# Kernel tuning notes

Measured on AMD Instinct MI355X. Metric: run time of the kernel, lower is better.

Reference implementation:

```python
import jax, jax.numpy as jnp
import numpy as np

SEQ, BATCH, IN_DIM, HID, OUT = 512, 256, 300, 256, 2


def setup_inputs() -> dict:
    key = jax.random.key(0)
    ks = jax.random.split(key, 7)
    s_ih = 1.0 / np.sqrt(HID)
    return {
        "x": jax.random.normal(ks[0], (SEQ, BATCH, IN_DIM), jnp.float32),
        "W_ih": jax.random.uniform(ks[1], (HID, IN_DIM), jnp.float32, -s_ih, s_ih),
        "W_hh": jax.random.uniform(ks[2], (HID, HID), jnp.float32, -s_ih, s_ih),
        "b_ih": jax.random.uniform(ks[3], (HID,), jnp.float32, -s_ih, s_ih),
        "b_hh": jax.random.uniform(ks[4], (HID,), jnp.float32, -s_ih, s_ih),
        "W_fc": jax.random.uniform(ks[5], (OUT, HID), jnp.float32, -s_ih, s_ih),
        "b_fc": jax.random.uniform(ks[6], (OUT,), jnp.float32, -s_ih, s_ih),
    }


def reference(x, W_ih, W_hh, b_ih, b_hh, W_fc, b_fc):
    # Precompute input projection for all timesteps at once: [T, B, H]
    xp = jnp.einsum('tbi,hi->tbh', x, W_ih) + b_ih + b_hh

    def step(h, xt):
        h_new = jnp.tanh(xt + h @ W_hh.T)
        return h_new, None

    h0 = jnp.zeros((x.shape[1], W_hh.shape[0]), x.dtype)
    hT, _ = jax.lax.scan(step, h0, xp)  # hT: [B, H]
    # Dropout(0.3) is identity in eval mode.
    logits = hT @ W_fc.T + b_fc  # [B, 2]
    return jax.nn.log_softmax(logits, axis=-1)
```

## Files before the change

kernel.cpp:

```cpp
#include <hip/hip_runtime.h>
#include <hip/hip_bf16.h>
#include <cstdint>
#include <cstddef>

#define SEQ 512
#define BATCH 256
#define IN_DIM 300
#define HID 256

typedef __attribute__((ext_vector_type(8))) short bf16x8;
typedef __attribute__((ext_vector_type(4))) float f32x4;

__device__ __forceinline__ float bitsf(unsigned int u) {
  union { unsigned int u; float f; } v; v.u = u; return v.f;
}
__device__ __forceinline__ unsigned int pk2(float a, float b) {
  union { __hip_bfloat162 h2; unsigned int u; } p;
  p.h2 = __float22bfloat162_rn(make_float2(a, b));
  return p.u;
}
__device__ __forceinline__ bf16x8 cvt8(float a0,float a1,float a2,float a3,
                                       float a4,float a5,float a6,float a7) {
  union { __hip_bfloat162 h2[4]; bf16x8 v; } c;
  c.h2[0] = __float22bfloat162_rn(make_float2(a0, a1));
  c.h2[1] = __float22bfloat162_rn(make_float2(a2, a3));
  c.h2[2] = __float22bfloat162_rn(make_float2(a4, a5));
  c.h2[3] = __float22bfloat162_rn(make_float2(a6, a7));
  return c.v;
}

__global__ __launch_bounds__(256) void gemm_xp(const float* __restrict__ x,
    const float* __restrict__ W_ih, const float* __restrict__ b_ih,
    const float* __restrict__ b_hh, unsigned int* __restrict__ xp2)
{
  __shared__ unsigned short a_lds[64][40];
  __shared__ unsigned short w_lds[256][40];
  const int tid  = threadIdx.x;
  const int wave = tid >> 6;
  const int lane = tid & 63;
  const int l15  = lane & 15;
  const int quad = lane >> 4;
  const long m0 = (long)blockIdx.x * 64;

  f32x4 acc[4][4];
  #pragma unroll
  for (int mt = 0; mt < 4; ++mt)
    #pragma unroll
    for (int nt = 0; nt < 4; ++nt) acc[mt][nt] = (f32x4){0.f, 0.f, 0.f, 0.f};

  const int ar = tid >> 2;
  const int ac = (tid & 3) * 8;

  float av[8];
  float4 wv[8];
  {
    const float* src = x + (size_t)(m0 + ar) * IN_DIM + ac;
    float2 p0 = *(const float2*)(src + 0);
    float2 p1 = *(const float2*)(src + 2);
    float2 p2 = *(const float2*)(src + 4);
    float2 p3 = *(const float2*)(src + 6);
    av[0]=p0.x; av[1]=p0.y; av[2]=p1.x; av[3]=p1.y;
    av[4]=p2.x; av[5]=p2.y; av[6]=p3.x; av[7]=p3.y;
    #pragma unroll
    for (int i = 0; i < 8; ++i) {
      int e = tid + i * 256;
      wv[i] = *(const float4*)(W_ih + (e >> 3) * IN_DIM + (e & 7) * 4);
    }
  }

  for (int kc = 0; kc < 10; ++kc) {
    *(bf16x8*)&a_lds[ar][ac] = cvt8(av[0],av[1],av[2],av[3],av[4],av[5],av[6],av[7]);
    #pragma unroll
    for (int i = 0; i < 8; ++i) {
      int e = tid + i * 256;
      union { unsigned int u[2]; uint2 d; } pk;
      pk.u[0] = pk2(wv[i].x, wv[i].y);
      pk.u[1] = pk2(wv[i].z, wv[i].w);
      *(uint2*)&w_lds[e >> 3][(e & 7) * 4] = pk.d;
    }
    __syncthreads();
    if (kc < 9) {
      const int k0 = (kc + 1) * 32;
      const float* src = x + (size_t)(m0 + ar) * IN_DIM + (k0 + ac);
      if (k0 + ac + 8 <= IN_DIM) {
        float2 p0 = *(const float2*)(src + 0);
        float2 p1 = *(const float2*)(src + 2);
        float2 p2 = *(const float2*)(src + 4);
        float2 p3 = *(const float2*)(src + 6);
        av[0]=p0.x; av[1]=p0.y; av[2]=p1.x; av[3]=p1.y;
        av[4]=p2.x; av[5]=p2.y; av[6]=p3.x; av[7]=p3.y;
      } else {
        #pragma unroll
        for (int j = 0; j < 8; ++j) av[j] = (k0 + ac + j < IN_DIM) ? src[j] : 0.f;
      }
      #pragma unroll
      for (int i = 0; i < 8; ++i) {
        int e = tid + i * 256;
        int kk = k0 + (e & 7) * 4;
        wv[i] = (kk + 4 <= IN_DIM)
              ? *(const float4*)(W_ih + (e >> 3) * IN_DIM + kk)
              : make_float4(0.f, 0.f, 0.f, 0.f);
      }
    }
    bf16x8 afr[4], bfr[4];
    #pragma unroll
    for (int mt = 0; mt < 4; ++mt)
      afr[mt] = *(const bf16x8*)&a_lds[mt*16 + l15][quad*8];
    #pragma unroll
    for (int nt = 0; nt < 4; ++nt)
      bfr[nt] = *(const bf16x8*)&w_lds[wave*64 + nt*16 + l15][quad*8];
    #pragma unroll
    for (int mt = 0; mt < 4; ++mt)
      #pragma unroll
      for (int nt = 0; nt < 4; ++nt)
        acc[mt][nt] = __builtin_amdgcn_mfma_f32_16x16x32_bf16(afr[mt], bfr[nt], acc[mt][nt], 0, 0, 0);
    __syncthreads();
  }
  const int t = (int)(blockIdx.x >> 2);
  const float kb0 = 2.0f * (b_ih[wave*64 +  0 + l15] + b_hh[wave*64 +  0 + l15]);
  const float kb1 = 2.0f * (b_ih[wave*64 + 16 + l15] + b_hh[wave*64 + 16 + l15]);
  const float kb2 = 2.0f * (b_ih[wave*64 + 32 + l15] + b_hh[wave*64 + 32 + l15]);
  const float kb3 = 2.0f * (b_ih[wave*64 + 48 + l15] + b_hh[wave*64 + 48 + l15]);
  #pragma unroll
  for (int mt = 0; mt < 4; ++mt) {
    const int g = ((int)(blockIdx.x & 3))*16 + mt*4 + quad;
    const size_t base = ((size_t)t*64 + g)*512;
    #pragma unroll
    for (int r = 0; r < 4; ++r) {
      unsigned int d0 = pk2(fmaf(2.0f, acc[mt][0][r], kb0), fmaf(2.0f, acc[mt][1][r], kb1));
      unsigned int d1 = pk2(fmaf(2.0f, acc[mt][2][r], kb2), fmaf(2.0f, acc[mt][3][r], kb3));
      xp2[base + (wave*2    )*64 + r*16 + l15] = d0;
      xp2[base + (wave*2 + 1)*64 + r*16 + l15] = d1;
    }
  }
}

__global__ __launch_bounds__(512) void rnn_scan(const float* __restrict__ W_hh,
    const unsigned int* __restrict__ xp2, float* __restrict__ hT)
{
  __shared__ alignas(16) unsigned short hbuf[2][4 * 272];
  const int tid  = threadIdx.x;
  const int wave = tid >> 6;
  const int lane = tid & 63;
  const int l15  = lane & 15;
  const int quad = lane >> 4;
  const int g = blockIdx.x;
  const int c0 = wave * 32;

  bf16x8 wf[2][8];
  #pragma unroll
  for (int nt = 0; nt < 2; ++nt) {
    const int n = c0 + nt*16 + l15;
    #pragma unroll
    for (int kc = 0; kc < 8; ++kc) {
      const float* src = W_hh + n*HID + kc*32 + quad*4;
      float4 p0 = *(const float4*)src;
      float4 p1 = *(const float4*)(src + 16);
      wf[nt][kc] = cvt8(p0.x,p1.x,p0.y,p1.y,p0.z,p1.z,p0.w,p1.w);
    }
  }

  const int abase = (l15 & 3) * 272 + quad * 8;
  const int wofs  = quad * 272 + wave * 32 + l15 * 2;

  for (int i = tid; i < 4 * 272; i += 512) hbuf[0][i] = 0;

  const unsigned int* xbase = xp2 + (size_t)g * 512 + tid;

  __syncthreads();

  unsigned int xq[32];
  for (int tc = 0; tc < SEQ / 32; ++tc) {
    const unsigned int* pb = xbase + (size_t)tc * 32 * 32768;
    #pragma unroll
    for (int j = 0; j < 32; ++j)
      xq[j] = pb[(size_t)j * 32768];
    #pragma unroll
    for (int j = 0; j < 32; ++j) {
      const int cur = j & 1;
      bf16x8 afr[8];
      #pragma unroll
      for (int kc = 0; kc < 8; ++kc)
        afr[kc] = *(const bf16x8*)&hbuf[cur][abase + kc*32];
      f32x4 c00 = (f32x4){0.f,0.f,0.f,0.f}, c01 = c00, c10 = c00, c11 = c00;
      #pragma unroll
      for (int kc = 0; kc < 8; kc += 2) {
        c00 = __builtin_amdgcn_mfma_f32_16x16x32_bf16(afr[kc],   wf[0][kc],   c00, 0, 0, 0);
        c10 = __builtin_amdgcn_mfma_f32_16x16x32_bf16(afr[kc],   wf[1][kc],   c10, 0, 0, 0);
        c01 = __builtin_amdgcn_mfma_f32_16x16x32_bf16(afr[kc+1], wf[0][kc+1], c01, 0, 0, 0);
        c11 = __builtin_amdgcn_mfma_f32_16x16x32_bf16(afr[kc+1], wf[1][kc+1], c11, 0, 0, 0);
      }
      const bool qb0 = (quad & 1) != 0, qb1 = (quad & 2) != 0;
      float a0 = qb1 ? (qb0 ? c00[3]+c01[3] : c00[2]+c01[2])
                     : (qb0 ? c00[1]+c01[1] : c00[0]+c01[0]);
      float a1 = qb1 ? (qb0 ? c10[3]+c11[3] : c10[2]+c11[2])
                     : (qb0 ? c10[1]+c11[1] : c10[0]+c11[0]);
      float xv0 = bitsf(xq[j] << 16);
      float xv1 = bitsf(xq[j] & 0xffff0000u);
      float y0 = fmaf(2.0f, a0, xv0);
      float y1 = fmaf(2.0f, a1, xv1);
      float h0 = fmaf(-2.0f, __builtin_amdgcn_rcpf(__expf(y0) + 1.0f), 1.0f);
      float h1 = fmaf(-2.0f, __builtin_amdgcn_rcpf(__expf(y1) + 1.0f), 1.0f);
      if (j < 31 || tc < SEQ/32 - 1) {
        *(unsigned int*)&hbuf[1 - cur][wofs] = pk2(h0, h1);
      } else {
        hT[(size_t)(g*4 + quad) * HID + c0 + l15]      = h0;
        hT[(size_t)(g*4 + quad) * HID + c0 + 16 + l15] = h1;
      }
      __syncthreads();
    }
  }
}

__global__ __launch_bounds__(64) void fc_head(const float* __restrict__ hT,
    const float* __restrict__ W_fc, const float* __restrict__ b_fc,
    float* __restrict__ out)
{
  const int b = blockIdx.x;
  const int l = threadIdx.x;
  float s0 = 0.f, s1 = 0.f;
  #pragma unroll
  for (int j0 = 0; j0 < HID; j0 += 64) {
    float h = hT[(size_t)b * HID + j0 + l];
    s0 += h * W_fc[j0 + l];
    s1 += h * W_fc[HID + j0 + l];
  }
  #pragma unroll
  for (int off = 32; off > 0; off >>= 1) {
    s0 += __shfl_xor(s0, off, 64);
    s1 += __shfl_xor(s1, off, 64);
  }
  if (l == 0) {
    float l0 = s0 + b_fc[0], l1 = s1 + b_fc[1];
    float m = fmaxf(l0, l1);
    float lse = m + logf(expf(l0 - m) + expf(l1 - m));
    out[b*2 + 0] = l0 - lse;
    out[b*2 + 1] = l1 - lse;
  }
}

extern "C" void kernel_launch(void* const* d_in, const int* in_sizes, int n_in,
                              void* d_out, int out_size, void* d_ws, size_t ws_size,
                              hipStream_t stream) {
  const float* x    = (const float*)d_in[0];
  const float* W_ih = (const float*)d_in[1];
  const float* W_hh = (const float*)d_in[2];
  const float* b_ih = (const float*)d_in[3];
  const float* b_hh = (const float*)d_in[4];
  const float* W_fc = (const float*)d_in[5];
  const float* b_fc = (const float*)d_in[6];
  float* out = (float*)d_out;

  const size_t xp_bytes = (size_t)SEQ * BATCH * HID * 2;
  const size_t ht_bytes = (size_t)BATCH * HID * 4;
  if (ws_size < xp_bytes + ht_bytes) return;

  char* ws = (char*)d_ws;
  unsigned int* xp2 = (unsigned int*)ws;
  float*        hT  = (float*)(ws + xp_bytes);

  hipLaunchKernelGGL(gemm_xp,  dim3(2048), dim3(256), 0, stream, x, W_ih, b_ih, b_hh, xp2);
  hipLaunchKernelGGL(rnn_scan, dim3(64),   dim3(512), 0, stream, W_hh, xp2, hT);
  hipLaunchKernelGGL(fc_head,  dim3(BATCH), dim3(64), 0, stream, hT, W_fc, b_fc, out);
}
```

Before: 509.4 us.

## Halve scan waves per block, four N-tiles per wave, pre-permuted bf16 W_hh

The recurrent scan now uses 4 waves of 256 threads instead of 8 waves of 512. Each wave computes 64 hidden columns using four N-tiles, and it loads 8-byte xp chunks and writes 8-byte h chunks to LDS. A new pre-kernel converts W_hh to bf16 in a permuted layout so the scan loads its weight fragments with single vector loads. The aim is to cut per-step barrier cost across fewer waves and widen memory accesses. In exchange each wave has a longer serial MFMA chain and higher register pressure (32 weight fragments).

```diff
diff --git a/kernel.cpp b/kernel.cpp
--- a/kernel.cpp
+++ b/kernel.cpp
@@ -13,6 +13,11 @@
 
 __device__ __forceinline__ float bitsf(unsigned int u) {
   union { unsigned int u; float f; } v; v.u = u; return v.f;
+}
+__device__ __forceinline__ unsigned short f2bf(float f) {
+  union { float f; unsigned int u; } v; v.f = f;
+  unsigned int u = v.u;
+  return (unsigned short)((u + 0x7fffu + ((u >> 16) & 1u)) >> 16);
 }
 __device__ __forceinline__ unsigned int pk2(float a, float b) {
   union { __hip_bfloat162 h2; unsigned int u; } p;
@@ -29,9 +34,17 @@
   return c.v;
 }
 
+__global__ __launch_bounds__(256) void conv_whh(const float* __restrict__ W_hh,
+                                                unsigned short* __restrict__ w_perm) {
+  int idx = blockIdx.x * 256 + threadIdx.x;
+  int n = idx >> 8, P = idx & 255;
+  int k = (P & 192) + 16 * (P & 3) + ((P >> 2) & 15);
+  w_perm[idx] = f2bf(W_hh[n * 256 + k]);
+}
+
 __global__ __launch_bounds__(256) void gemm_xp(const float* __restrict__ x,
     const float* __restrict__ W_ih, const float* __restrict__ b_ih,
-    const float* __restrict__ b_hh, unsigned int* __restrict__ xp2)
+    const float* __restrict__ b_hh, uint2* __restrict__ xpv)
 {
   __shared__ unsigned short a_lds[64][40];
   __shared__ unsigned short w_lds[256][40];
@@ -124,88 +137,91 @@
   #pragma unroll
   for (int mt = 0; mt < 4; ++mt) {
     const int g = ((int)(blockIdx.x & 3))*16 + mt*4 + quad;
-    const size_t base = ((size_t)t*64 + g)*512;
+    const size_t base = ((size_t)t*64 + g)*256;
     #pragma unroll
     for (int r = 0; r < 4; ++r) {
-      unsigned int d0 = pk2(fmaf(2.0f, acc[mt][0][r], kb0), fmaf(2.0f, acc[mt][1][r], kb1));
-      unsigned int d1 = pk2(fmaf(2.0f, acc[mt][2][r], kb2), fmaf(2.0f, acc[mt][3][r], kb3));
-      xp2[base + (wave*2    )*64 + r*16 + l15] = d0;
-      xp2[base + (wave*2 + 1)*64 + r*16 + l15] = d1;
-    }
-  }
-}
-
-__global__ __launch_bounds__(512) void rnn_scan(const float* __restrict__ W_hh,
-    const unsigned int* __restrict__ xp2, float* __restrict__ hT)
+      uint2 d;
+      d.x = pk2(fmaf(2.0f, acc[mt][0][r], kb0), fmaf(2.0f, acc[mt][1][r], kb1));
+      d.y = pk2(fmaf(2.0f, acc[mt][2][r], kb2), fmaf(2.0f, acc[mt][3][r], kb3));
+      xpv[base + wave*64 + r*16 + l15] = d;
+    }
+  }
+}
+
+__global__ __launch_bounds__(256, 1) void rnn_scan(
+    const unsigned short* __restrict__ w_perm,
+    const uint2* __restrict__ xpv, float* __restrict__ hT)
 {
-  __shared__ alignas(16) unsigned short hbuf[2][4 * 272];
+  __shared__ alignas(16) unsigned short hbuf[2][4][272];
   const int tid  = threadIdx.x;
   const int wave = tid >> 6;
   const int lane = tid & 63;
   const int l15  = lane & 15;
   const int quad = lane >> 4;
   const int g = blockIdx.x;
-  const int c0 = wave * 32;
-
-  bf16x8 wf[2][8];
-  #pragma unroll
-  for (int nt = 0; nt < 2; ++nt) {
+  const int c0 = wave * 64;
+  const int m = l15 & 3;
+
+  bf16x8 wf[4][8];
+  #pragma unroll
+  for (int nt = 0; nt < 4; ++nt) {
     const int n = c0 + nt*16 + l15;
     #pragma unroll
-    for (int kc = 0; kc < 8; ++kc) {
-      const float* src = W_hh + n*HID + kc*32 + quad*4;
-      float4 p0 = *(const float4*)src;
-      float4 p1 = *(const float4*)(src + 16);
-      wf[nt][kc] = cvt8(p0.x,p1.x,p0.y,p1.y,p0.z,p1.z,p0.w,p1.w);
-    }
-  }
-
-  const int abase = (l15 & 3) * 272 + quad * 8;
-  const int wofs  = quad * 272 + wave * 32 + l15 * 2;
-
-  for (int i = tid; i < 4 * 272; i += 512) hbuf[0][i] = 0;
-
-  const unsigned int* xbase = xp2 + (size_t)g * 512 + tid;
+    for (int kc = 0; kc < 8; ++kc)
+      wf[nt][kc] = *(const bf16x8*)(w_perm + (size_t)n*256 + kc*32 + quad*8);
+  }
+
+  for (int i = tid; i < 4 * 272; i += 256) (&hbuf[0][0][0])[i] = 0;
+
+  const uint2* xb = xpv + (size_t)g * 256 + tid;
 
   __syncthreads();
 
-  unsigned int xq[32];
-  for (int tc = 0; tc < SEQ / 32; ++tc) {
-    const unsigned int* pb = xbase + (size_t)tc * 32 * 32768;
-    #pragma unroll
-    for (int j = 0; j < 32; ++j)
-      xq[j] = pb[(size_t)j * 32768];
-    #pragma unroll
-    for (int j = 0; j < 32; ++j) {
+  uint2 xq[16];
+  for (int tc = 0; tc < SEQ / 16; ++tc) {
+    #pragma unroll
+    for (int j = 0; j < 16; ++j)
+      xq[j] = xb[(size_t)(tc * 16 + j) * 16384];
+    #pragma unroll
+    for (int j = 0; j < 16; ++j) {
       const int cur = j & 1;
       bf16x8 afr[8];
       #pragma unroll
       for (int kc = 0; kc < 8; ++kc)
-        afr[kc] = *(const bf16x8*)&hbuf[cur][abase + kc*32];
-      f32x4 c00 = (f32x4){0.f,0.f,0.f,0.f}, c01 = c00, c10 = c00, c11 = c00;
+        afr[kc] = *(const bf16x8*)&hbuf[cur][m][kc*32 + quad*8];
+      f32x4 cA[4], cB[4];
+      #pragma unroll
+      for (int nt = 0; nt < 4; ++nt) { cA[nt] = (f32x4){0.f,0.f,0.f,0.f}; cB[nt] = cA[nt]; }
       #pragma unroll
       for (int kc = 0; kc < 8; kc += 2) {
-        c00 = __builtin_amdgcn_mfma_f32_16x16x32_bf16(afr[kc],   wf[0][kc],   c00, 0, 0, 0);
-        c10 = __builtin_amdgcn_mfma_f32_16x16x32_bf16(afr[kc],   wf[1][kc],   c10, 0, 0, 0);
-        c01 = __builtin_amdgcn_mfma_f32_16x16x32_bf16(afr[kc+1], wf[0][kc+1], c01, 0, 0, 0);
-        c11 = __builtin_amdgcn_mfma_f32_16x16x32_bf16(afr[kc+1], wf[1][kc+1], c11, 0, 0, 0);
-      }
-      const bool qb0 = (quad & 1) != 0, qb1 = (quad & 2) != 0;
-      float a0 = qb1 ? (qb0 ? c00[3]+c01[3] : c00[2]+c01[2])
-                     : (qb0 ? c00[1]+c01[1] : c00[0]+c01[0]);
-      float a1 = qb1 ? (qb0 ? c10[3]+c11[3] : c10[2]+c11[2])
-                     : (qb0 ? c10[1]+c11[1] : c10[0]+c11[0]);
-      float xv0 = bitsf(xq[j] << 16);
-      float xv1 = bitsf(xq[j] & 0xffff0000u);
-      float y0 = fmaf(2.0f, a0, xv0);
-      float y1 = fmaf(2.0f, a1, xv1);
-      float h0 = fmaf(-2.0f, __builtin_amdgcn_rcpf(__expf(y0) + 1.0f), 1.0f);
-      float h1 = fmaf(-2.0f, __builtin_amdgcn_rcpf(__expf(y1) + 1.0f), 1.0f);
-      if (j < 31 || tc < SEQ/32 - 1) {
-        *(unsigned int*)&hbuf[1 - cur][wofs] = pk2(h0, h1);
+        #pragma unroll
+        for (int nt = 0; nt < 4; ++nt) {
+          cA[nt] = __builtin_amdgcn_mfma_f32_16x16x32_bf16(afr[kc],   wf[nt][kc],   cA[nt], 0, 0, 0);
+          cB[nt] = __builtin_amdgcn_mfma_f32_16x16x32_bf16(afr[kc+1], wf[nt][kc+1], cB[nt], 0, 0, 0);
+        }
+      }
+      float xv[4], h[4];
+      xv[0] = bitsf(xq[j].x << 16);
+      xv[1] = bitsf(xq[j].x & 0xffff0000u);
+      xv[2] = bitsf(xq[j].y << 16);
+      xv[3] = bitsf(xq[j].y & 0xffff0000u);
+      #pragma unroll
+      for (int nt = 0; nt < 4; ++nt) {
+        f32x4 s = cA[nt] + cB[nt];
+        float a = (quad & 2) ? ((quad & 1) ? s[3] : s[2])
+                             : ((quad & 1) ? s[1] : s[0]);
+        float y = fmaf(2.0f, a, xv[nt]);
+        h[nt] = fmaf(-2.0f, __builtin_amdgcn_rcpf(__expf(y) + 1.0f), 1.0f);
+      }
+      if (j < 15 || tc < SEQ/16 - 1) {
+        uint2 w2;
+        w2.x = pk2(h[0], h[1]);
+        w2.y = pk2(h[2], h[3]);
+        *(uint2*)&hbuf[1 - cur][quad][wave*64 + l15*4] = w2;
       } else {
-        hT[(size_t)(g*4 + quad) * HID + c0 + l15]      = h0;
-        hT[(size_t)(g*4 + quad) * HID + c0 + 16 + l15] = h1;
+        #pragma unroll
+        for (int nt = 0; nt < 4; ++nt)
+          hT[(size_t)(g*4 + quad) * HID + c0 + nt*16 + l15] = h[nt];
       }
       __syncthreads();
     }
@@ -252,14 +268,17 @@
   float* out = (float*)d_out;
 
   const size_t xp_bytes = (size_t)SEQ * BATCH * HID * 2;
+  const size_t wp_bytes = (size_t)256 * 256 * 2;
   const size_t ht_bytes = (size_t)BATCH * HID * 4;
-  if (ws_size < xp_bytes + ht_bytes) return;
+  if (ws_size < xp_bytes + wp_bytes + ht_bytes) return;
 
   char* ws = (char*)d_ws;
-  unsigned int* xp2 = (unsigned int*)ws;
-  float*        hT  = (float*)(ws + xp_bytes);
-
-  hipLaunchKernelGGL(gemm_xp,  dim3(2048), dim3(256), 0, stream, x, W_ih, b_ih, b_hh, xp2);
-  hipLaunchKernelGGL(rnn_scan, dim3(64),   dim3(512), 0, stream, W_hh, xp2, hT);
+  uint2*          xpv    = (uint2*)ws;
+  unsigned short* w_perm = (unsigned short*)(ws + xp_bytes);
+  float*          hT     = (float*)(ws + xp_bytes + wp_bytes);
+
+  hipLaunchKernelGGL(conv_whh, dim3(256),  dim3(256), 0, stream, W_hh, w_perm);
+  hipLaunchKernelGGL(gemm_xp,  dim3(2048), dim3(256), 0, stream, x, W_ih, b_ih, b_hh, xpv);
+  hipLaunchKernelGGL(rnn_scan, dim3(64),   dim3(256), 0, stream, w_perm, xpv, hT);
   hipLaunchKernelGGL(fc_head,  dim3(BATCH), dim3(64), 0, stream, hT, W_fc, b_fc, out);
 }
```

New measurement: 566.2 us. 11.2% more time.
